# Performance work log

Hardware: AMD Instinct MI355X
Metric: run time of the kernel (lower is better)

## Reference

```python
import jax, jax.numpy as jnp
import numpy as np

B, L, D, H = 1, 4096, 1024, 16
HD = D // H  # head dim = 64
WINDOW = 15


def _rope(t, cos, sin):
    # t: [B,H,L,HD]; cos/sin: [1,1,L,HD//2]
    tr = t.reshape(*t.shape[:-1], HD // 2, 2)
    a, b = tr[..., 0], tr[..., 1]
    out_r = a * cos - b * sin
    out_i = a * sin + b * cos
    return jnp.stack([out_r, out_i], axis=-1).reshape(t.shape)


def _longformer_mask(L, window):
    i = jnp.arange(L)[:, None]
    j = jnp.arange(L)[None, :]
    causal = j <= i
    win = jnp.abs(i - j) <= window // 2
    glob = (j == 0) | (i == 0)
    return (causal & win) | glob  # [L,L] bool


def setup_inputs() -> dict:
    key = jax.random.key(0)
    kx, kq, kk, kv, ko = jax.random.split(key, 5)
    x = jax.random.normal(kx, (B, L, D), dtype=jnp.float32)
    scale = 0.02
    Wq = jax.random.normal(kq, (D, D), dtype=jnp.float32) * scale
    Wk = jax.random.normal(kk, (D, D), dtype=jnp.float32) * scale
    Wv = jax.random.normal(kv, (D, D), dtype=jnp.float32) * scale
    Wo = jax.random.normal(ko, (D, D), dtype=jnp.float32) * scale
    # real RoPE frequencies (complex freqs_cis split into cos/sin)
    inv_freq = 1.0 / (10000.0 ** (np.arange(0, HD, 2, dtype=np.float32) / HD))
    pos = np.arange(L, dtype=np.float32)
    ang = pos[:, None] * inv_freq[None, :]  # [L, HD//2]
    freqs_cos = jnp.asarray(np.cos(ang))[None]  # [1,L,HD//2]
    freqs_sin = jnp.asarray(np.sin(ang))[None]
    return {"x": x, "Wq": Wq, "Wk": Wk, "Wv": Wv, "Wo": Wo,
            "freqs_cos": freqs_cos, "freqs_sin": freqs_sin}


def reference(x, Wq, Wk, Wv, Wo, freqs_cos, freqs_sin):
    b, l, _ = x.shape
    # projections (nn.Linear: y = x @ W^T)
    Q = (x @ Wq.T).reshape(b, l, H, HD).transpose(0, 2, 1, 3)  # [B,H,L,HD]
    K = (x @ Wk.T).reshape(b, l, H, HD).transpose(0, 2, 1, 3)
    V = (x @ Wv.T).reshape(b, l, H, HD).transpose(0, 2, 1, 3)
    cos = freqs_cos[:, None, :l]  # [1,1,L,HD//2] (torch unsqueeze(1))
    sin = freqs_sin[:, None, :l]
    Q = _rope(Q, cos, sin)
    K = _rope(K, cos, sin)
    mask = _longformer_mask(l, WINDOW)  # [L,L]
    scores = jnp.einsum('bhqd,bhkd->bhqk', Q, K) / jnp.sqrt(jnp.float32(HD))
    scores = jnp.where(mask[None, None], scores, jnp.finfo(scores.dtype).min)
    attn = jax.nn.softmax(scores, axis=-1)
    out = jnp.einsum('bhqk,bhkd->bhqd', attn, V)  # [B,H,L,HD]
    out = out.transpose(0, 2, 1, 3).reshape(b, l, D)
    return out @ Wo.T
```

## Files before the change

kernel.cpp:

```cpp
#include <hip/hip_runtime.h>
#include <stdint.h>

#define SL 4096
#define DM 1024
#define NH 16
#define HDIM 64

typedef short short8 __attribute__((ext_vector_type(8)));
typedef float f32x4 __attribute__((ext_vector_type(4)));

__device__ __forceinline__ unsigned short f2bf(float f) {
  unsigned int u = __float_as_uint(f);
  u += 0x7FFF + ((u >> 16) & 1);
  return (unsigned short)(u >> 16);
}
__device__ __forceinline__ float bf2f(unsigned short u) {
  return __uint_as_float((unsigned int)u << 16);
}
__device__ __forceinline__ float bflo(unsigned int u) { return __uint_as_float(u << 16); }
__device__ __forceinline__ float bfhi(unsigned int u) { return __uint_as_float(u & 0xffff0000u); }

__device__ __forceinline__ void gload_lds16(const void* g, void* l) {
  __builtin_amdgcn_global_load_lds((const __attribute__((address_space(1))) void*)g,
                                   (__attribute__((address_space(3))) void*)l, 16, 0, 0);
}
#define SBAR()                                  \
  do {                                          \
    __builtin_amdgcn_sched_barrier(0);          \
    __builtin_amdgcn_s_barrier();               \
    __builtin_amdgcn_sched_barrier(0);          \
  } while (0)
#define LGKM0() asm volatile("s_waitcnt lgkmcnt(0)" ::: "memory")

__global__ void cast_all(const float* __restrict__ x,
                         const float* __restrict__ Wq, const float* __restrict__ Wk,
                         const float* __restrict__ Wv, const float* __restrict__ Wo,
                         unsigned short* __restrict__ xb,
                         unsigned short* __restrict__ w3b, unsigned short* __restrict__ wob) {
  int i = blockIdx.x * blockDim.x + threadIdx.x;
  const float* src;
  unsigned short* dst;
  int off;
  if (i < (1 << 20)) {
    src = x; dst = xb; off = i;
  } else {
    int wsel = i - (1 << 20);
    int seg = wsel >> 18;
    off = wsel & 262143;
    src = (seg == 0) ? Wq : (seg == 1) ? Wk : (seg == 2) ? Wv : Wo;
    dst = (seg < 3) ? (w3b + (size_t)seg * DM * DM) : wob;
  }
  float4 v = ((const float4*)src)[off];
  ushort4 o = make_ushort4(f2bf(v.x), f2bf(v.y), f2bf(v.z), f2bf(v.w));
  ((ushort4*)dst)[off] = o;
}

__global__ __launch_bounds__(512, 4)
void gemm1_rope(const unsigned short* __restrict__ A,
                const unsigned short* __restrict__ B,
                unsigned short* __restrict__ C,
                const float* __restrict__ fc, const float* __restrict__ fs) {
  constexpr int K = 1024, LDA = 1024, LDC = 3072, NT = K / 64;
  __shared__ __align__(16) unsigned short As[2][128 * 64];
  __shared__ __align__(16) unsigned short Bs[2][192 * 64];
  const int tid = threadIdx.x, w = tid >> 6, lane = tid & 63;
  const int wr = w >> 2, wc = w & 3;

  const int gx = gridDim.x;
  const int total = gx * gridDim.y;
  const int lin = blockIdx.y * gx + blockIdx.x;
  const int swz = (lin & 7) * (total >> 3) + (lin >> 3);
  const int brow = (swz / gx) * 128;
  const int bcol = (swz % gx) * 192;

  const unsigned short* gA[2];
  const unsigned short* gB[3];
#pragma unroll
  for (int l = 0; l < 2; ++l) {
    int idx = l * 512 + tid;
    int row_l = idx >> 3, c = idx & 7;
    int csrc = c ^ ((row_l >> 1) & 7);
    gA[l] = A + (size_t)(brow + row_l) * LDA + csrc * 8;
  }
#pragma unroll
  for (int l = 0; l < 3; ++l) {
    int idx = l * 512 + tid;
    int row_l = idx >> 3, c = idx & 7;
    int csrc = c ^ ((row_l >> 1) & 7);
    gB[l] = B + (size_t)(bcol + row_l) * LDA + csrc * 8;
  }

  auto STG_A = [&](int t) {
    const int buf = t & 1;
#pragma unroll
    for (int l = 0; l < 2; ++l)
      gload_lds16(gA[l] + t * 64, &As[buf][(l * 512 + w * 64) * 8]);
  };
  auto STG_B_a = [&](int t) {
    const int buf = t & 1;
#pragma unroll
    for (int l = 0; l < 2; ++l)
      gload_lds16(gB[l] + t * 64, &Bs[buf][(l * 512 + w * 64) * 8]);
  };
  auto STG_B_b = [&](int t) {
    const int buf = t & 1;
    gload_lds16(gB[2] + t * 64, &Bs[buf][(2 * 512 + w * 64) * 8]);
  };

  const int lrow = lane & 15, h4 = lane >> 4;
  const int g3 = (lane >> 1) & 7;
  const int u2 = h4 ^ (g3 & 3);
  const int gv = g3 >> 2;
  const int co0 = ((((0 ^ gv) << 2) | u2)) * 8;
  const int co1 = ((((1 ^ gv) << 2) | u2)) * 8;

  f32x4 acc[4][3] = {};
  short8 a0[4], a1[4], b0[3], b1[3];

  STG_A(0); STG_B_a(0); STG_B_b(0);
  STG_A(1); STG_B_a(1); STG_B_b(1);
  asm volatile("s_waitcnt vmcnt(5)" ::: "memory");
  SBAR();

  for (int t = 0; t < NT; ++t) {
    const int buf = t & 1;
    const unsigned short* Ab = &As[buf][(wr * 64 + lrow) * 64];
    const unsigned short* Bb = &Bs[buf][(wc * 48 + lrow) * 64];
#pragma unroll
    for (int n = 0; n < 3; ++n) b0[n] = *(const short8*)&Bb[n * 16 * 64 + co0];
#pragma unroll
    for (int m = 0; m < 4; ++m) a0[m] = *(const short8*)&Ab[m * 16 * 64 + co0];
    SBAR();
    __builtin_amdgcn_s_setprio(1);
#pragma unroll
    for (int m = 0; m < 4; ++m)
#pragma unroll
      for (int n = 0; n < 3; ++n)
        acc[m][n] = __builtin_amdgcn_mfma_f32_16x16x32_bf16(a0[m], b0[n], acc[m][n], 0, 0, 0);
    __builtin_amdgcn_s_setprio(0);
#pragma unroll
    for (int n = 0; n < 3; ++n) b1[n] = *(const short8*)&Bb[n * 16 * 64 + co1];
#pragma unroll
    for (int m = 0; m < 4; ++m) a1[m] = *(const short8*)&Ab[m * 16 * 64 + co1];
    LGKM0();
    SBAR();
    __builtin_amdgcn_s_setprio(1);
#pragma unroll
    for (int m = 0; m < 4; ++m)
      acc[m][0] = __builtin_amdgcn_mfma_f32_16x16x32_bf16(a1[m], b1[0], acc[m][0], 0, 0, 0);
    __builtin_amdgcn_s_setprio(0);
    if (t + 2 < NT) STG_A(t + 2);
    SBAR();
    __builtin_amdgcn_s_setprio(1);
#pragma unroll
    for (int m = 0; m < 4; ++m)
      acc[m][1] = __builtin_amdgcn_mfma_f32_16x16x32_bf16(a1[m], b1[1], acc[m][1], 0, 0, 0);
    __builtin_amdgcn_s_setprio(0);
    if (t + 2 < NT) { STG_B_a(t + 2); STG_B_b(t + 2); }
    if (t >= NT - 2) {
      asm volatile("s_waitcnt vmcnt(0)" ::: "memory");
    } else {
      asm volatile("s_waitcnt vmcnt(5)" ::: "memory");
    }
    SBAR();
    __builtin_amdgcn_s_setprio(1);
#pragma unroll
    for (int m = 0; m < 4; ++m)
      acc[m][2] = __builtin_amdgcn_mfma_f32_16x16x32_bf16(a1[m], b1[2], acc[m][2], 0, 0, 0);
    __builtin_amdgcn_s_setprio(0);
  }

  const int er = (lane >> 4) * 4;
  const int ec = lane & 15;
#pragma unroll
  for (int n = 0; n < 3; ++n) {
    if (bcol + wc * 48 + n * 16 < 2048) {
      const int p = ((wc * 48 + n * 16 + ec) & 63) >> 1;
#pragma unroll
      for (int m = 0; m < 4; ++m) {
#pragma unroll
        for (int r = 0; r < 4; ++r) {
          const int row = brow + wr * 64 + m * 16 + er + r;
          float v = acc[m][n][r];
          float pv = __shfl_xor(v, 1);
          float cs = fc[row * 32 + p], sn = fs[row * 32 + p];
          acc[m][n][r] = (lane & 1) ? (pv * sn + v * cs) : (v * cs - pv * sn);
        }
      }
    }
  }
#pragma unroll
  for (int m = 0; m < 4; ++m)
#pragma unroll
    for (int n = 0; n < 3; ++n) {
      unsigned short* cp = C + (size_t)(brow + wr * 64 + m * 16 + er) * LDC +
                           (bcol + wc * 48 + n * 16 + ec);
#pragma unroll
      for (int r = 0; r < 4; ++r) cp[(size_t)r * LDC] = f2bf(acc[m][n][r]);
    }
}

__global__ __launch_bounds__(512)
void gemm2_4ph(const unsigned short* __restrict__ A,
               const unsigned short* __restrict__ B,
               float* __restrict__ C) {
  constexpr int K = 1024, LDA = 1024, LDC = 1024, NT = K / 64;
  __shared__ __align__(16) unsigned short As2[2][128 * 64];
  __shared__ __align__(16) unsigned short Bs2[2][128 * 64];
  const int tid = threadIdx.x, w = tid >> 6, lane = tid & 63;
  const int wr = w >> 2, wc = w & 3;

  const int gx = gridDim.x;
  const int total = gx * gridDim.y;
  const int lin = blockIdx.y * gx + blockIdx.x;
  const int swz = (lin & 7) * (total >> 3) + (lin >> 3);
  const int brow = (swz / gx) * 128;
  const int bcol = (swz % gx) * 128;

  const unsigned short* gA[2];
  const unsigned short* gB[2];
#pragma unroll
  for (int l = 0; l < 2; ++l) {
    int idx = l * 512 + tid;
    int row_l = idx >> 3, c = idx & 7;
    int csrc = c ^ ((row_l >> 1) & 7);
    gA[l] = A + (size_t)(brow + row_l) * LDA + csrc * 8;
    gB[l] = B + (size_t)(bcol + row_l) * LDA + csrc * 8;
  }

  auto STG_A = [&](int t, int h) {
    const int buf = t & 1;
    gload_lds16(gA[h] + t * 64, &As2[buf][(h * 512 + w * 64) * 8]);
  };
  auto STG_B = [&](int t, int h) {
    const int buf = t & 1;
    gload_lds16(gB[h] + t * 64, &Bs2[buf][(h * 512 + w * 64) * 8]);
  };

  const int lrow = lane & 15, h4 = lane >> 4;
  const int g3 = (lane >> 1) & 7;
  const int u2 = h4 ^ (g3 & 3);
  const int gv = g3 >> 2;
  const int co0 = ((((0 ^ gv) << 2) | u2)) * 8;
  const int co1 = ((((1 ^ gv) << 2) | u2)) * 8;

  f32x4 acc[4][2] = {};
  short8 a0[4], a1[4], b0[2], b1[2];

  STG_A(0, 0); STG_A(0, 1); STG_B(0, 0); STG_B(0, 1);
  STG_A(1, 0); STG_A(1, 1); STG_B(1, 0); STG_B(1, 1);
  asm volatile("s_waitcnt vmcnt(4)" ::: "memory");
  SBAR();

  for (int t = 0; t < NT; ++t) {
    const int buf = t & 1;
    const unsigned short* Ab = &As2[buf][(wr * 64 + lrow) * 64];
    const unsigned short* Bb = &Bs2[buf][(wc * 32 + lrow) * 64];
#pragma unroll
    for (int n = 0; n < 2; ++n) b0[n] = *(const short8*)&Bb[n * 16 * 64 + co0];
#pragma unroll
    for (int m = 0; m < 4; ++m) a0[m] = *(const short8*)&Ab[m * 16 * 64 + co0];
    SBAR();
    __builtin_amdgcn_s_setprio(1);
#pragma unroll
    for (int m = 0; m < 4; ++m)
      acc[m][0] = __builtin_amdgcn_mfma_f32_16x16x32_bf16(a0[m], b0[0], acc[m][0], 0, 0, 0);
    __builtin_amdgcn_s_setprio(0);
#pragma unroll
    for (int n = 0; n < 2; ++n) b1[n] = *(const short8*)&Bb[n * 16 * 64 + co1];
#pragma unroll
    for (int m = 0; m < 4; ++m) a1[m] = *(const short8*)&Ab[m * 16 * 64 + co1];
    LGKM0();
    SBAR();
    __builtin_amdgcn_s_setprio(1);
#pragma unroll
    for (int m = 0; m < 4; ++m)
      acc[m][1] = __builtin_amdgcn_mfma_f32_16x16x32_bf16(a0[m], b0[1], acc[m][1], 0, 0, 0);
    __builtin_amdgcn_s_setprio(0);
    if (t + 2 < NT) { STG_A(t + 2, 0); STG_B(t + 2, 0); }
    SBAR();
    __builtin_amdgcn_s_setprio(1);
#pragma unroll
    for (int m = 0; m < 4; ++m)
      acc[m][0] = __builtin_amdgcn_mfma_f32_16x16x32_bf16(a1[m], b1[0], acc[m][0], 0, 0, 0);
    __builtin_amdgcn_s_setprio(0);
    if (t + 2 < NT) { STG_A(t + 2, 1); STG_B(t + 2, 1); }
    if (t >= NT - 2) {
      asm volatile("s_waitcnt vmcnt(0)" ::: "memory");
    } else {
      asm volatile("s_waitcnt vmcnt(4)" ::: "memory");
    }
    SBAR();
    __builtin_amdgcn_s_setprio(1);
#pragma unroll
    for (int m = 0; m < 4; ++m)
      acc[m][1] = __builtin_amdgcn_mfma_f32_16x16x32_bf16(a1[m], b1[1], acc[m][1], 0, 0, 0);
    __builtin_amdgcn_s_setprio(0);
  }

  const int er = (lane >> 4) * 4;
  const int ec = lane & 15;
#pragma unroll
  for (int m = 0; m < 4; ++m)
#pragma unroll
    for (int n = 0; n < 2; ++n) {
      float* cp = C + (size_t)(brow + wr * 64 + m * 16 + er) * LDC +
                  (bcol + wc * 32 + n * 16 + ec);
#pragma unroll
      for (int r = 0; r < 4; ++r) cp[(size_t)r * LDC] = acc[m][n][r];
    }
}

__global__ __launch_bounds__(256)
void attn_fused(const unsigned short* __restrict__ qkv, unsigned short* __restrict__ atb,
                float* __restrict__ prt) {
  const int wid = threadIdx.x >> 6;
  const int lane = threadIdx.x & 63;
  if (blockIdx.x >= 1024) {
    const int u = (blockIdx.x - 1024) * 4 + wid;
    const int p = u & 127, h = u >> 7;
    const float q = bf2f(qkv[h * 64 + lane]);
    float m = -1e30f, s = 0.f, o = 0.f;
    const int j0 = p * 32;
    for (int jj = 0; jj < 32; ++jj) {
      const int j = j0 + jj;
      float kv = bf2f(qkv[(size_t)j * 3072 + 1024 + h * 64 + lane]);
      float pr = q * kv;
#pragma unroll
      for (int off = 32; off; off >>= 1) pr += __shfl_xor(pr, off);
      pr *= 0.125f;
      float mn = fmaxf(m, pr);
      float c = __expf(m - mn);
      float e = __expf(pr - mn);
      float v = bf2f(qkv[(size_t)j * 3072 + 2048 + h * 64 + lane]);
      s = s * c + e;
      o = o * c + e * v;
      m = mn;
    }
    float* dst = prt + ((size_t)h * 128 + p) * 72;
    if (lane == 0) { dst[0] = m; dst[1] = s; }
    dst[2 + lane] = o;
    return;
  }

  const int i = blockIdx.x * 4 + wid + 1;
  if (i >= SL) return;
  const unsigned short* rowQ = qkv + (size_t)i * 3072 + lane * 16;

  float q[16];
  {
    uint4 a = *(const uint4*)rowQ;
    uint4 b = *(const uint4*)(rowQ + 8);
    unsigned int uu[8] = {a.x, a.y, a.z, a.w, b.x, b.y, b.z, b.w};
#pragma unroll
    for (int c = 0; c < 8; ++c) { q[2 * c] = bflo(uu[c]); q[2 * c + 1] = bfhi(uu[c]); }
  }

  float sc[9];
#pragma unroll
  for (int t = 0; t < 9; ++t) {
    int j = (t == 0) ? 0 : (i - 8 + t);
    bool valid = (t == 0) || (j >= 1);
    int jc = valid ? j : 0;
    const unsigned short* pk = qkv + (size_t)jc * 3072 + 1024 + lane * 16;
    uint4 a = *(const uint4*)pk;
    uint4 b = *(const uint4*)(pk + 8);
    unsigned int uu[8] = {a.x, a.y, a.z, a.w, b.x, b.y, b.z, b.w};
    float pr = 0.f;
#pragma unroll
    for (int c = 0; c < 8; ++c) pr += bflo(uu[c]) * q[2 * c] + bfhi(uu[c]) * q[2 * c + 1];
    pr += __shfl_xor(pr, 1);
    pr += __shfl_xor(pr, 2);
    sc[t] = valid ? pr * 0.125f : -1e30f;
  }

  float mx = sc[0];
#pragma unroll
  for (int t = 1; t < 9; ++t) mx = fmaxf(mx, sc[t]);
  float s = 0.f;
#pragma unroll
  for (int t = 0; t < 9; ++t) { float e = __expf(sc[t] - mx); sc[t] = e; s += e; }
  const float inv = 1.0f / s;

  float o[16] = {};
#pragma unroll
  for (int t = 0; t < 9; ++t) {
    int j = (t == 0) ? 0 : (i - 8 + t);
    bool valid = (t == 0) || (j >= 1);
    int jc = valid ? j : 0;
    const unsigned short* pv = qkv + (size_t)jc * 3072 + 2048 + lane * 16;
    uint4 a = *(const uint4*)pv;
    uint4 b = *(const uint4*)(pv + 8);
    unsigned int uu[8] = {a.x, a.y, a.z, a.w, b.x, b.y, b.z, b.w};
#pragma unroll
    for (int c = 0; c < 8; ++c) {
      o[2 * c]     += sc[t] * bflo(uu[c]);
      o[2 * c + 1] += sc[t] * bfhi(uu[c]);
    }
  }

  unsigned int wv[8];
#pragma unroll
  for (int c = 0; c < 8; ++c)
    wv[c] = (unsigned int)f2bf(o[2 * c] * inv) | ((unsigned int)f2bf(o[2 * c + 1] * inv) << 16);
  unsigned short* po = atb + (size_t)i * 1024 + lane * 16;
  uint4 s0; s0.x = wv[0]; s0.y = wv[1]; s0.z = wv[2]; s0.w = wv[3];
  uint4 s1; s1.x = wv[4]; s1.y = wv[5]; s1.z = wv[6]; s1.w = wv[7];
  *(uint4*)po = s0;
  *(uint4*)(po + 8) = s1;
}

__global__ __launch_bounds__(64)
void attn_row0_combine(const float* __restrict__ prt, unsigned short* __restrict__ atb) {
  const int h = blockIdx.x;
  const int lane = threadIdx.x;
  const float* base = prt + (size_t)h * 128 * 72;
  __shared__ float cbuf[128];
  float m0 = base[lane * 72];
  float m1 = base[(lane + 64) * 72];
  float M = fmaxf(m0, m1);
#pragma unroll
  for (int off = 32; off; off >>= 1) M = fmaxf(M, __shfl_xor(M, off));
  float c0 = __expf(m0 - M), c1 = __expf(m1 - M);
  float ls = base[lane * 72 + 1] * c0 + base[(lane + 64) * 72 + 1] * c1;
#pragma unroll
  for (int off = 32; off; off >>= 1) ls += __shfl_xor(ls, off);
  cbuf[lane] = c0;
  cbuf[lane + 64] = c1;
  __syncthreads();
  float o = 0.f;
#pragma unroll 8
  for (int p = 0; p < 128; ++p) o += cbuf[p] * base[p * 72 + 2 + lane];
  atb[h * 64 + lane] = f2bf(o / ls);
}

extern "C" void kernel_launch(void* const* d_in, const int* in_sizes, int n_in,
                              void* d_out, int out_size, void* d_ws, size_t ws_size,
                              hipStream_t stream) {
  const float* x  = (const float*)d_in[0];
  const float* Wq = (const float*)d_in[1];
  const float* Wk = (const float*)d_in[2];
  const float* Wv = (const float*)d_in[3];
  const float* Wo = (const float*)d_in[4];
  const float* fc = (const float*)d_in[5];
  const float* fs = (const float*)d_in[6];
  float* out = (float*)d_out;

  char* ws = (char*)d_ws;
  unsigned short* xb   = (unsigned short*)(ws);
  unsigned short* w3b  = (unsigned short*)(ws + ((size_t)8 << 20));
  unsigned short* wob  = (unsigned short*)(ws + ((size_t)14 << 20));
  unsigned short* qkvb = (unsigned short*)(ws + ((size_t)16 << 20));
  unsigned short* atb  = (unsigned short*)(ws + ((size_t)40 << 20));
  float*          prt  = (float*)(ws + ((size_t)48 << 20));

  cast_all<<<(2 * (1 << 20)) / 256, 256, 0, stream>>>(x, Wq, Wk, Wv, Wo, xb, w3b, wob);

  dim3 g1(3072 / 192, SL / 128);
  gemm1_rope<<<g1, 512, 0, stream>>>(xb, w3b, qkvb, fc, fs);

  attn_fused<<<1536, 256, 0, stream>>>(qkvb, atb, prt);
  attn_row0_combine<<<NH, 64, 0, stream>>>(prt, atb);

  dim3 g2(DM / 128, SL / 128);
  gemm2_4ph<<<g2, 512, 0, stream>>>(atb, wob, out);
}
```

Before: 88.32 us.

## Load output-projection B operand directly into registers, staging only A in LDS

The output-projection GEMM no longer stages the weight (B) tile through shared memory. Each wave loads its B fragments straight from global memory into registers, double-buffered across iterations. The A tile still goes through double-buffered LDS, but the four-phase barrier and priority schedule is replaced by one barrier per K-step. This halves LDS use and removes the LDS read traffic for B, at the cost of uncoalesced-ish global reads for B, less latency hiding than the deeper two-ahead prefetch, and reliance on the barrier to wait for the async LDS loads.

```diff
diff --git a/kernel.cpp b/kernel.cpp
--- a/kernel.cpp
+++ b/kernel.cpp
@@ -201,12 +201,11 @@
 }
 
 __global__ __launch_bounds__(512)
-void gemm2_4ph(const unsigned short* __restrict__ A,
-               const unsigned short* __restrict__ B,
-               float* __restrict__ C) {
+void gemm2_bd(const unsigned short* __restrict__ A,
+              const unsigned short* __restrict__ B,
+              float* __restrict__ C) {
   constexpr int K = 1024, LDA = 1024, LDC = 1024, NT = K / 64;
   __shared__ __align__(16) unsigned short As2[2][128 * 64];
-  __shared__ __align__(16) unsigned short Bs2[2][128 * 64];
   const int tid = threadIdx.x, w = tid >> 6, lane = tid & 63;
   const int wr = w >> 2, wc = w & 3;
 
@@ -218,26 +217,29 @@
   const int bcol = (swz % gx) * 128;
 
   const unsigned short* gA[2];
-  const unsigned short* gB[2];
 #pragma unroll
   for (int l = 0; l < 2; ++l) {
     int idx = l * 512 + tid;
     int row_l = idx >> 3, c = idx & 7;
     int csrc = c ^ ((row_l >> 1) & 7);
     gA[l] = A + (size_t)(brow + row_l) * LDA + csrc * 8;
-    gB[l] = B + (size_t)(bcol + row_l) * LDA + csrc * 8;
-  }
-
-  auto STG_A = [&](int t, int h) {
-    const int buf = t & 1;
-    gload_lds16(gA[h] + t * 64, &As2[buf][(h * 512 + w * 64) * 8]);
-  };
-  auto STG_B = [&](int t, int h) {
-    const int buf = t & 1;
-    gload_lds16(gB[h] + t * 64, &Bs2[buf][(h * 512 + w * 64) * 8]);
+  }
+  auto STG_A = [&](int t, int buf) {
+#pragma unroll
+    for (int l = 0; l < 2; ++l)
+      gload_lds16(gA[l] + t * 64, &As2[buf][(l * 512 + w * 64) * 8]);
   };
 
   const int lrow = lane & 15, h4 = lane >> 4;
+  const unsigned short* gBf = B + (size_t)(bcol + wc * 32 + lrow) * LDA + h4 * 8;
+  auto LOADB = [&](short8* d, int t) {
+#pragma unroll
+    for (int n = 0; n < 2; ++n)
+#pragma unroll
+      for (int ks = 0; ks < 2; ++ks)
+        d[n * 2 + ks] = *(const short8*)(gBf + (size_t)n * 16 * LDA + t * 64 + ks * 32);
+  };
+
   const int g3 = (lane >> 1) & 7;
   const int u2 = h4 ^ (g3 & 3);
   const int gv = g3 >> 2;
@@ -245,57 +247,32 @@
   const int co1 = ((((1 ^ gv) << 2) | u2)) * 8;
 
   f32x4 acc[4][2] = {};
-  short8 a0[4], a1[4], b0[2], b1[2];
-
-  STG_A(0, 0); STG_A(0, 1); STG_B(0, 0); STG_B(0, 1);
-  STG_A(1, 0); STG_A(1, 1); STG_B(1, 0); STG_B(1, 1);
-  asm volatile("s_waitcnt vmcnt(4)" ::: "memory");
-  SBAR();
-
-  for (int t = 0; t < NT; ++t) {
+  short8 bA[4], bB[4];
+
+  auto BODY = [&](int t, short8* bcur, short8* bnxt) {
     const int buf = t & 1;
+    __syncthreads();
+    if (t + 1 < NT) { STG_A(t + 1, buf ^ 1); LOADB(bnxt, t + 1); }
     const unsigned short* Ab = &As2[buf][(wr * 64 + lrow) * 64];
-    const unsigned short* Bb = &Bs2[buf][(wc * 32 + lrow) * 64];
-#pragma unroll
-    for (int n = 0; n < 2; ++n) b0[n] = *(const short8*)&Bb[n * 16 * 64 + co0];
+    short8 a0[4], a1[4];
 #pragma unroll
     for (int m = 0; m < 4; ++m) a0[m] = *(const short8*)&Ab[m * 16 * 64 + co0];
-    SBAR();
-    __builtin_amdgcn_s_setprio(1);
+#pragma unroll
+    for (int m = 0; m < 4; ++m) a1[m] = *(const short8*)&Ab[m * 16 * 64 + co1];
 #pragma unroll
     for (int m = 0; m < 4; ++m)
-      acc[m][0] = __builtin_amdgcn_mfma_f32_16x16x32_bf16(a0[m], b0[0], acc[m][0], 0, 0, 0);
-    __builtin_amdgcn_s_setprio(0);
-#pragma unroll
-    for (int n = 0; n < 2; ++n) b1[n] = *(const short8*)&Bb[n * 16 * 64 + co1];
-#pragma unroll
-    for (int m = 0; m < 4; ++m) a1[m] = *(const short8*)&Ab[m * 16 * 64 + co1];
-    LGKM0();
-    SBAR();
-    __builtin_amdgcn_s_setprio(1);
-#pragma unroll
-    for (int m = 0; m < 4; ++m)
-      acc[m][1] = __builtin_amdgcn_mfma_f32_16x16x32_bf16(a0[m], b0[1], acc[m][1], 0, 0, 0);
-    __builtin_amdgcn_s_setprio(0);
-    if (t + 2 < NT) { STG_A(t + 2, 0); STG_B(t + 2, 0); }
-    SBAR();
-    __builtin_amdgcn_s_setprio(1);
-#pragma unroll
-    for (int m = 0; m < 4; ++m)
-      acc[m][0] = __builtin_amdgcn_mfma_f32_16x16x32_bf16(a1[m], b1[0], acc[m][0], 0, 0, 0);
-    __builtin_amdgcn_s_setprio(0);
-    if (t + 2 < NT) { STG_A(t + 2, 1); STG_B(t + 2, 1); }
-    if (t >= NT - 2) {
-      asm volatile("s_waitcnt vmcnt(0)" ::: "memory");
-    } else {
-      asm volatile("s_waitcnt vmcnt(4)" ::: "memory");
-    }
-    SBAR();
-    __builtin_amdgcn_s_setprio(1);
-#pragma unroll
-    for (int m = 0; m < 4; ++m)
-      acc[m][1] = __builtin_amdgcn_mfma_f32_16x16x32_bf16(a1[m], b1[1], acc[m][1], 0, 0, 0);
-    __builtin_amdgcn_s_setprio(0);
+#pragma unroll
+      for (int n = 0; n < 2; ++n) {
+        acc[m][n] = __builtin_amdgcn_mfma_f32_16x16x32_bf16(a0[m], bcur[n * 2 + 0], acc[m][n], 0, 0, 0);
+        acc[m][n] = __builtin_amdgcn_mfma_f32_16x16x32_bf16(a1[m], bcur[n * 2 + 1], acc[m][n], 0, 0, 0);
+      }
+  };
+
+  STG_A(0, 0);
+  LOADB(bA, 0);
+  for (int t = 0; t < NT; t += 2) {
+    BODY(t, bA, bB);
+    BODY(t + 1, bB, bA);
   }
 
   const int er = (lane >> 4) * 4;
@@ -463,5 +440,5 @@
   attn_row0_combine<<<NH, 64, 0, stream>>>(prt, atb);
 
   dim3 g2(DM / 128, SL / 128);
-  gemm2_4ph<<<g2, 512, 0, stream>>>(atb, wob, out);
-}
+  gemm2_bd<<<g2, 512, 0, stream>>>(atb, wob, out);
+}
```

Measured after the change: 96.09 us. +8.8%, slower.
